# Optimization experiments

Measured on AMD Instinct MI355X. Metric: run time of the kernel, lower is better.

The kernel has to match this reference:

```python
import jax, jax.numpy as jnp
import numpy as np

TOP_K = 2


def setup_inputs() -> dict:
    key = jax.random.key(0)
    k1, k2, k3, k4 = jax.random.split(key, 4)
    B, T, D = 1, 2048, 1024
    E, F = 8, 2048
    scale_in = 1.0 / np.sqrt(D)
    scale_f = 1.0 / np.sqrt(F)
    x = jax.random.normal(k1, (B, T, D), dtype=jnp.float32)
    Wr = jax.random.normal(k2, (E, D), dtype=jnp.float32) * scale_in  # router weight [E, D]
    W1 = jax.random.normal(k3, (E, F, D), dtype=jnp.float32) * scale_in  # fc1 weights stacked [E, F, D]
    W2 = jax.random.normal(k4, (E, D, F), dtype=jnp.float32) * scale_f  # fc2 weights stacked [E, D, F]
    return {"x": x, "Wr": Wr, "W1": W1, "W2": W2}


def reference(x, Wr, W1, W2):
    B, T, D = x.shape
    E = Wr.shape[0]
    xf = x.reshape(B * T, D)  # [N, D]
    N = xf.shape[0]

    # Router: softmax over experts, top-k gating, renormalized
    logits = xf @ Wr.T  # [N, E]
    probs = jax.nn.softmax(logits, axis=-1)
    top_vals, top_idx = jax.lax.top_k(probs, TOP_K)  # [N, K]
    top_vals = top_vals / jnp.sum(top_vals, axis=-1, keepdims=True)

    # Dense per-token gate matrix: gates[n, e] = sum_k top_vals[n,k] * (top_idx[n,k]==e)
    gates = jnp.zeros((N, E), dtype=x.dtype).at[
        jnp.arange(N)[:, None], top_idx
    ].add(top_vals)  # [N, E]

    # Expert MLP: fc2(relu(fc1(x))^2), computed densely for all experts then
    # combined with the (mostly-zero) gate weights.
    h = jnp.einsum("nd,efd->nef", xf, W1)  # [N, E, F]
    a = jnp.square(jax.nn.relu(h))
    y = jnp.einsum("nef,edf->ned", a, W2)  # [N, E, D]
    out = jnp.einsum("ne,ned->nd", gates, y)  # [N, D]
    return out.reshape(B, T, D)
```

## Files before the change

### kernel.cpp

```cpp
#include <hip/hip_runtime.h>
#include <hip/hip_bf16.h>
#include <cstdint>
#include <cstddef>

#define N_TOK 2048
#define DIM   1024
#define NEXP  8
#define FDIM  2048

#define BM 128
#define BN 128
#define BK 64

typedef __attribute__((ext_vector_type(8))) short short8;
typedef __attribute__((ext_vector_type(4))) float f32x4;
typedef unsigned short ushort_t;

#define OFF_COUNTS  0
#define OFF_TOK     4096
#define OFF_GATE    (OFF_TOK + NEXP * N_TOK * 4)
#define OFF_A       ((size_t)1 << 20)
#define OFF_W1B     (OFF_A  + (size_t)2 * N_TOK * FDIM * 2)
#define OFF_W2B     (OFF_W1B + (size_t)NEXP * FDIM * DIM * 2)
#define OFF_XB      (OFF_W2B + (size_t)NEXP * DIM * FDIM * 2)

__device__ __forceinline__ uint32_t cvt2(float lo, float hi) {
  __hip_bfloat162 p = __float22bfloat162_rn(make_float2(lo, hi));
  uint32_t r; __builtin_memcpy(&r, &p, 4); return r;
}

__device__ __forceinline__ void gl16(const ushort_t* g, const ushort_t* l) {
  __builtin_amdgcn_global_load_lds(
      (const __attribute__((address_space(1))) void*)g,
      (__attribute__((address_space(3))) void*)l, 16, 0, 0);
}

__device__ __forceinline__ int xcd_swz(int bid, int nwg) {
  int q = nwg >> 3, r = nwg & 7;
  int xcd = bid & 7, local = bid >> 3;
  int base = (xcd < r) ? xcd * (q + 1) : r * (q + 1) + (xcd - r) * q;
  return base + local;
}

__global__ __launch_bounds__(256) void prep_kernel(
    const float* __restrict__ W1, const float* __restrict__ W2, const float* __restrict__ x,
    ushort_t* __restrict__ W1b, ushort_t* __restrict__ W2b, ushort_t* __restrict__ xb) {
  int b = blockIdx.x;
  const float* s; ushort_t* d; size_t off;
  if (b < 1024)      { s = W1; d = W1b; off = (size_t)b * 16384; }
  else if (b < 2048) { s = W2; d = W2b; off = (size_t)(b - 1024) * 16384; }
  else               { s = x;  d = xb;  off = (size_t)(b - 2048) * 16384; }
  s += off; d += off;
  int t8 = threadIdx.x * 8;
#pragma unroll
  for (int j = 0; j < 8; ++j) {
    float4 f0 = *(const float4*)(s + j * 2048 + t8);
    float4 f1 = *(const float4*)(s + j * 2048 + t8 + 4);
    *(uint4*)(d + j * 2048 + t8) =
        make_uint4(cvt2(f0.x, f0.y), cvt2(f0.z, f0.w), cvt2(f1.x, f1.y), cvt2(f1.z, f1.w));
  }
}

__global__ __launch_bounds__(256) void router_kernel(
    const float* __restrict__ x, const float* __restrict__ Wr,
    int* __restrict__ counts, int* __restrict__ toklist,
    float* __restrict__ gatelist) {
  int n = blockIdx.x * 4 + (threadIdx.x >> 6);
  int lane = threadIdx.x & 63;
  const float* xr = x + (size_t)n * DIM;

  float xv[DIM / 64];
#pragma unroll
  for (int i = 0; i < DIM / 64; ++i) xv[i] = xr[lane + 64 * i];

  float logit[NEXP];
#pragma unroll
  for (int e = 0; e < NEXP; ++e) {
    const float* wr = Wr + (size_t)e * DIM;
    float s = 0.f;
#pragma unroll
    for (int i = 0; i < DIM / 64; ++i) s += xv[i] * wr[lane + 64 * i];
#pragma unroll
    for (int off = 32; off; off >>= 1) s += __shfl_down(s, off);
    logit[e] = s;
  }

  if (lane == 0) {
    float m = logit[0];
#pragma unroll
    for (int e = 1; e < NEXP; ++e) m = fmaxf(m, logit[e]);
    float p[NEXP];
#pragma unroll
    for (int e = 0; e < NEXP; ++e) p[e] = expf(logit[e] - m);
    int i1 = 0;
#pragma unroll
    for (int e = 1; e < NEXP; ++e) if (p[e] > p[i1]) i1 = e;
    int i2 = (i1 == 0) ? 1 : 0;
#pragma unroll
    for (int e = 0; e < NEXP; ++e)
      if (e != i1 && p[e] > p[i2]) i2 = e;
    float denom = p[i1] + p[i2];

    int pos1 = atomicAdd(&counts[i1], 1);
    toklist[i1 * N_TOK + pos1] = n;
    gatelist[i1 * N_TOK + pos1] = p[i1] / denom;

    int pos2 = atomicAdd(&counts[i2], 1);
    toklist[i2 * N_TOK + pos2] = n;
    gatelist[i2 * N_TOK + pos2] = p[i2] / denom;
  }
}

__global__ __launch_bounds__(256, 3) void fc1_mfma(
    const ushort_t* __restrict__ xb, const ushort_t* __restrict__ W1b,
    const int* __restrict__ counts, const int* __restrict__ toklist,
    __hip_bfloat16* __restrict__ Abuf) {
  const int ROWB = N_TOK / BM;
  const int COLB = FDIM / BN;
  int bid = xcd_swz(blockIdx.x, NEXP * ROWB * COLB);
  int e  = bid / (ROWB * COLB);
  int rb = (bid / COLB) % ROWB;
  int cb = bid % COLB;
  int ne = counts[e];
  if (rb * BM >= ne) return;
  int base = 0;
  for (int i = 0; i < e; ++i) base += counts[i];

  __shared__ ushort_t As[BM * BK];
  __shared__ ushort_t Bs[BN * BK];

  int tid = threadIdx.x, lane = tid & 63, w = tid >> 6;

  const ushort_t* gA[4]; const ushort_t* gB[4];
  const ushort_t* lA[4]; const ushort_t* lB[4];
#pragma unroll
  for (int i = 0; i < 4; ++i) {
    int row = w * 32 + i * 8 + (lane >> 3);
    int c16 = (lane & 7) ^ (row & 7);
    int r = rb * BM + row; if (r >= ne) r = ne - 1;
    int tok = toklist[e * N_TOK + r];
    gA[i] = xb + (size_t)tok * DIM + c16 * 8;
    gB[i] = W1b + ((size_t)e * FDIM + cb * BN + row) * DIM + c16 * 8;
    lA[i] = &As[w * 2048 + i * 512];
    lB[i] = &Bs[w * 2048 + i * 512];
  }

  int wr = (w >> 1) * 64, wc = (w & 1) * 64;
  int lr = lane & 15, lg = lane >> 4;
  f32x4 acc[4][4] = {};

  for (int t = 0; t < DIM / BK; ++t) {
    __syncthreads();
#pragma unroll
    for (int i = 0; i < 4; ++i) {
      gl16(gA[i], lA[i]); gl16(gB[i], lB[i]);
      gA[i] += BK; gB[i] += BK;
    }
    __syncthreads();
#pragma unroll
    for (int ks = 0; ks < 2; ++ks) {
      short8 af[4], bf[4];
#pragma unroll
      for (int m = 0; m < 4; ++m) {
        int row = wr + m * 16 + lr;
        af[m] = *(const short8*)&As[row * BK + (((ks * 4 + lg) ^ (row & 7)) * 8)];
      }
#pragma unroll
      for (int n = 0; n < 4; ++n) {
        int row = wc + n * 16 + lr;
        bf[n] = *(const short8*)&Bs[row * BK + (((ks * 4 + lg) ^ (row & 7)) * 8)];
      }
#pragma unroll
      for (int m = 0; m < 4; ++m)
#pragma unroll
        for (int n = 0; n < 4; ++n)
          acc[m][n] = __builtin_amdgcn_mfma_f32_16x16x32_bf16(af[m], bf[n], acc[m][n], 0, 0, 0);
    }
  }

  int colbase = cb * BN + wc + lr;
#pragma unroll
  for (int m = 0; m < 4; ++m) {
#pragma unroll
    for (int j = 0; j < 4; ++j) {
      int r = rb * BM + wr + m * 16 + lg * 4 + j;
      if (r < ne) {
        __hip_bfloat16* orow = Abuf + (size_t)(base + r) * FDIM + colbase;
#pragma unroll
        for (int n = 0; n < 4; ++n) {
          float v = fmaxf(acc[m][n][j], 0.f);
          orow[n * 16] = __float2bfloat16(v * v);
        }
      }
    }
  }
}

__global__ __launch_bounds__(256, 3) void fc2_mfma(
    const ushort_t* __restrict__ Abuf, const ushort_t* __restrict__ W2b,
    const int* __restrict__ counts, const int* __restrict__ toklist,
    const float* __restrict__ gatelist, float* __restrict__ out) {
  const int ROWB = N_TOK / BM;
  const int COLB = DIM / BN;
  int bid = xcd_swz(blockIdx.x, NEXP * ROWB * COLB);
  int e  = bid / (ROWB * COLB);
  int rb = (bid / COLB) % ROWB;
  int cb = bid % COLB;
  int ks0 = blockIdx.y * (FDIM / 2);
  int ne = counts[e];
  if (rb * BM >= ne) return;
  int base = 0;
  for (int i = 0; i < e; ++i) base += counts[i];

  __shared__ ushort_t As[BM * BK];
  __shared__ ushort_t Bs[BN * BK];

  int tid = threadIdx.x, lane = tid & 63, w = tid >> 6;

  const ushort_t* gA[4]; const ushort_t* gB[4];
  const ushort_t* lA[4]; const ushort_t* lB[4];
#pragma unroll
  for (int i = 0; i < 4; ++i) {
    int row = w * 32 + i * 8 + (lane >> 3);
    int c16 = (lane & 7) ^ (row & 7);
    int r = rb * BM + row; if (r >= ne) r = ne - 1;
    gA[i] = Abuf + (size_t)(base + r) * FDIM + ks0 + c16 * 8;
    gB[i] = W2b + ((size_t)e * DIM + cb * BN + row) * FDIM + ks0 + c16 * 8;
    lA[i] = &As[w * 2048 + i * 512];
    lB[i] = &Bs[w * 2048 + i * 512];
  }

  int wr = (w >> 1) * 64, wc = (w & 1) * 64;
  int lr = lane & 15, lg = lane >> 4;
  f32x4 acc[4][4] = {};

  for (int t = 0; t < (FDIM / 2) / BK; ++t) {
    __syncthreads();
#pragma unroll
    for (int i = 0; i < 4; ++i) {
      gl16(gA[i], lA[i]); gl16(gB[i], lB[i]);
      gA[i] += BK; gB[i] += BK;
    }
    __syncthreads();
#pragma unroll
    for (int ks = 0; ks < 2; ++ks) {
      short8 af[4], bf[4];
#pragma unroll
      for (int m = 0; m < 4; ++m) {
        int row = wr + m * 16 + lr;
        af[m] = *(const short8*)&As[row * BK + (((ks * 4 + lg) ^ (row & 7)) * 8)];
      }
#pragma unroll
      for (int n = 0; n < 4; ++n) {
        int row = wc + n * 16 + lr;
        bf[n] = *(const short8*)&Bs[row * BK + (((ks * 4 + lg) ^ (row & 7)) * 8)];
      }
#pragma unroll
      for (int m = 0; m < 4; ++m)
#pragma unroll
        for (int n = 0; n < 4; ++n)
          acc[m][n] = __builtin_amdgcn_mfma_f32_16x16x32_bf16(af[m], bf[n], acc[m][n], 0, 0, 0);
    }
  }

  int colbase = cb * BN + wc + lr;
#pragma unroll
  for (int m = 0; m < 4; ++m) {
#pragma unroll
    for (int j = 0; j < 4; ++j) {
      int r = rb * BM + wr + m * 16 + lg * 4 + j;
      if (r < ne) {
        int tok = toklist[e * N_TOK + r];
        float g = gatelist[e * N_TOK + r];
        float* orow = out + (size_t)tok * DIM + colbase;
#pragma unroll
        for (int n = 0; n < 4; ++n)
          atomicAdd(&orow[n * 16], g * acc[m][n][j]);
      }
    }
  }
}

extern "C" void kernel_launch(void* const* d_in, const int* in_sizes, int n_in,
                              void* d_out, int out_size, void* d_ws, size_t ws_size,
                              hipStream_t stream) {
  const float* x  = (const float*)d_in[0];
  const float* Wr = (const float*)d_in[1];
  const float* W1 = (const float*)d_in[2];
  const float* W2 = (const float*)d_in[3];
  float* out = (float*)d_out;

  char* ws = (char*)d_ws;
  int*   counts   = (int*)(ws + OFF_COUNTS);
  int*   toklist  = (int*)(ws + OFF_TOK);
  float* gatelist = (float*)(ws + OFF_GATE);
  __hip_bfloat16* Abuf = (__hip_bfloat16*)(ws + OFF_A);
  ushort_t* W1b = (ushort_t*)(ws + OFF_W1B);
  ushort_t* W2b = (ushort_t*)(ws + OFF_W2B);
  ushort_t* xb  = (ushort_t*)(ws + OFF_XB);

  (void)hipMemsetAsync(counts, 0, NEXP * sizeof(int), stream);
  (void)hipMemsetAsync(out, 0, (size_t)out_size * sizeof(float), stream);

  prep_kernel<<<2176, 256, 0, stream>>>(W1, W2, x, W1b, W2b, xb);

  router_kernel<<<N_TOK / 4, 256, 0, stream>>>(x, Wr, counts, toklist, gatelist);

  fc1_mfma<<<NEXP * (N_TOK / BM) * (FDIM / BN), 256, 0, stream>>>(
      xb, W1b, counts, toklist, Abuf);

  fc2_mfma<<<dim3(NEXP * (N_TOK / BM) * (DIM / BN), 2), 256, 0, stream>>>(
      (const ushort_t*)Abuf, W2b, counts, toklist, gatelist, out);
}
```

Baseline: 295.5 us.

## Double-buffer LDS in expert GEMMs and split weight conversion into smaller blocks

Both fc1 and fc2 GEMM kernels now use two LDS buffers. The next K-tile is loaded asynchronously with global_load_lds while the current one is consumed, using explicit vmcnt waits and raw barriers instead of two __syncthreads per iteration. This is meant to hide global-load latency behind MFMA work, at the cost of doubling LDS per block, and the occupancy hint drops from 3 to 2 blocks. The fp32-to-bf16 prep kernel is also reorganized into twice as many blocks with nontemporal vector loads and 8-byte stores, aiming for better streaming bandwidth on the large weight conversion.

```diff
diff --git a/kernel.cpp b/kernel.cpp
--- a/kernel.cpp
+++ b/kernel.cpp
@@ -14,6 +14,7 @@
 
 typedef __attribute__((ext_vector_type(8))) short short8;
 typedef __attribute__((ext_vector_type(4))) float f32x4;
+typedef __attribute__((ext_vector_type(2))) unsigned int uint2v;
 typedef unsigned short ushort_t;
 
 #define OFF_COUNTS  0
@@ -46,18 +47,19 @@
     const float* __restrict__ W1, const float* __restrict__ W2, const float* __restrict__ x,
     ushort_t* __restrict__ W1b, ushort_t* __restrict__ W2b, ushort_t* __restrict__ xb) {
   int b = blockIdx.x;
-  const float* s; ushort_t* d; size_t off;
-  if (b < 1024)      { s = W1; d = W1b; off = (size_t)b * 16384; }
-  else if (b < 2048) { s = W2; d = W2b; off = (size_t)(b - 1024) * 16384; }
-  else               { s = x;  d = xb;  off = (size_t)(b - 2048) * 16384; }
+  const f32x4* s; uint2v* d; size_t off;
+  if (b < 2048)      { s = (const f32x4*)W1; d = (uint2v*)W1b; off = (size_t)b * 2048; }
+  else if (b < 4096) { s = (const f32x4*)W2; d = (uint2v*)W2b; off = (size_t)(b - 2048) * 2048; }
+  else               { s = (const f32x4*)x;  d = (uint2v*)xb;  off = (size_t)(b - 4096) * 2048; }
   s += off; d += off;
-  int t8 = threadIdx.x * 8;
-#pragma unroll
-  for (int j = 0; j < 8; ++j) {
-    float4 f0 = *(const float4*)(s + j * 2048 + t8);
-    float4 f1 = *(const float4*)(s + j * 2048 + t8 + 4);
-    *(uint4*)(d + j * 2048 + t8) =
-        make_uint4(cvt2(f0.x, f0.y), cvt2(f0.z, f0.w), cvt2(f1.x, f1.y), cvt2(f1.z, f1.w));
+  int tid = threadIdx.x;
+  f32x4 v[8];
+#pragma unroll
+  for (int k = 0; k < 8; ++k) v[k] = __builtin_nontemporal_load(&s[tid + k * 256]);
+#pragma unroll
+  for (int k = 0; k < 8; ++k) {
+    uint2v o; o.x = cvt2(v[k].x, v[k].y); o.y = cvt2(v[k].z, v[k].w);
+    d[tid + k * 256] = o;
   }
 }
 
@@ -111,7 +113,7 @@
   }
 }
 
-__global__ __launch_bounds__(256, 3) void fc1_mfma(
+__global__ __launch_bounds__(256, 2) void fc1_mfma(
     const ushort_t* __restrict__ xb, const ushort_t* __restrict__ W1b,
     const int* __restrict__ counts, const int* __restrict__ toklist,
     __hip_bfloat16* __restrict__ Abuf) {
@@ -126,13 +128,12 @@
   int base = 0;
   for (int i = 0; i < e; ++i) base += counts[i];
 
-  __shared__ ushort_t As[BM * BK];
-  __shared__ ushort_t Bs[BN * BK];
+  __shared__ ushort_t As[2][BM * BK];
+  __shared__ ushort_t Bs[2][BN * BK];
 
   int tid = threadIdx.x, lane = tid & 63, w = tid >> 6;
 
   const ushort_t* gA[4]; const ushort_t* gB[4];
-  const ushort_t* lA[4]; const ushort_t* lB[4];
 #pragma unroll
   for (int i = 0; i < 4; ++i) {
     int row = w * 32 + i * 8 + (lane >> 3);
@@ -141,34 +142,41 @@
     int tok = toklist[e * N_TOK + r];
     gA[i] = xb + (size_t)tok * DIM + c16 * 8;
     gB[i] = W1b + ((size_t)e * FDIM + cb * BN + row) * DIM + c16 * 8;
-    lA[i] = &As[w * 2048 + i * 512];
-    lB[i] = &Bs[w * 2048 + i * 512];
   }
 
   int wr = (w >> 1) * 64, wc = (w & 1) * 64;
   int lr = lane & 15, lg = lane >> 4;
   f32x4 acc[4][4] = {};
 
-  for (int t = 0; t < DIM / BK; ++t) {
-    __syncthreads();
-#pragma unroll
-    for (int i = 0; i < 4; ++i) {
-      gl16(gA[i], lA[i]); gl16(gB[i], lB[i]);
-      gA[i] += BK; gB[i] += BK;
-    }
-    __syncthreads();
+#define ISSUE(buf, t) do { _Pragma("unroll") for (int i = 0; i < 4; ++i) { \
+    gl16(gA[i] + (size_t)(t) * BK, &As[buf][w * 2048 + i * 512]); \
+    gl16(gB[i] + (size_t)(t) * BK, &Bs[buf][w * 2048 + i * 512]); } } while (0)
+
+  const int NT = DIM / BK;
+  asm volatile("s_waitcnt vmcnt(0)" ::: "memory");
+  ISSUE(0, 0);
+  for (int t = 0; t < NT; ++t) {
+    int cur = t & 1;
+    if (t + 1 < NT) {
+      ISSUE(cur ^ 1, t + 1);
+      asm volatile("s_waitcnt vmcnt(8)" ::: "memory");
+    } else {
+      asm volatile("s_waitcnt vmcnt(0)" ::: "memory");
+    }
+    __builtin_amdgcn_sched_barrier(0);
+    __builtin_amdgcn_s_barrier();
 #pragma unroll
     for (int ks = 0; ks < 2; ++ks) {
       short8 af[4], bf[4];
 #pragma unroll
       for (int m = 0; m < 4; ++m) {
         int row = wr + m * 16 + lr;
-        af[m] = *(const short8*)&As[row * BK + (((ks * 4 + lg) ^ (row & 7)) * 8)];
+        af[m] = *(const short8*)&As[cur][row * BK + (((ks * 4 + lg) ^ (row & 7)) * 8)];
       }
 #pragma unroll
       for (int n = 0; n < 4; ++n) {
         int row = wc + n * 16 + lr;
-        bf[n] = *(const short8*)&Bs[row * BK + (((ks * 4 + lg) ^ (row & 7)) * 8)];
+        bf[n] = *(const short8*)&Bs[cur][row * BK + (((ks * 4 + lg) ^ (row & 7)) * 8)];
       }
 #pragma unroll
       for (int m = 0; m < 4; ++m)
@@ -176,7 +184,11 @@
         for (int n = 0; n < 4; ++n)
           acc[m][n] = __builtin_amdgcn_mfma_f32_16x16x32_bf16(af[m], bf[n], acc[m][n], 0, 0, 0);
     }
-  }
+    asm volatile("s_waitcnt lgkmcnt(0)" ::: "memory");
+    __builtin_amdgcn_sched_barrier(0);
+    __builtin_amdgcn_s_barrier();
+  }
+#undef ISSUE
 
   int colbase = cb * BN + wc + lr;
 #pragma unroll
@@ -196,7 +208,7 @@
   }
 }
 
-__global__ __launch_bounds__(256, 3) void fc2_mfma(
+__global__ __launch_bounds__(256, 2) void fc2_mfma(
     const ushort_t* __restrict__ Abuf, const ushort_t* __restrict__ W2b,
     const int* __restrict__ counts, const int* __restrict__ toklist,
     const float* __restrict__ gatelist, float* __restrict__ out) {
@@ -212,13 +224,12 @@
   int base = 0;
   for (int i = 0; i < e; ++i) base += counts[i];
 
-  __shared__ ushort_t As[BM * BK];
-  __shared__ ushort_t Bs[BN * BK];
+  __shared__ ushort_t As[2][BM * BK];
+  __shared__ ushort_t Bs[2][BN * BK];
 
   int tid = threadIdx.x, lane = tid & 63, w = tid >> 6;
 
   const ushort_t* gA[4]; const ushort_t* gB[4];
-  const ushort_t* lA[4]; const ushort_t* lB[4];
 #pragma unroll
   for (int i = 0; i < 4; ++i) {
     int row = w * 32 + i * 8 + (lane >> 3);
@@ -226,34 +237,41 @@
     int r = rb * BM + row; if (r >= ne) r = ne - 1;
     gA[i] = Abuf + (size_t)(base + r) * FDIM + ks0 + c16 * 8;
     gB[i] = W2b + ((size_t)e * DIM + cb * BN + row) * FDIM + ks0 + c16 * 8;
-    lA[i] = &As[w * 2048 + i * 512];
-    lB[i] = &Bs[w * 2048 + i * 512];
   }
 
   int wr = (w >> 1) * 64, wc = (w & 1) * 64;
   int lr = lane & 15, lg = lane >> 4;
   f32x4 acc[4][4] = {};
 
-  for (int t = 0; t < (FDIM / 2) / BK; ++t) {
-    __syncthreads();
-#pragma unroll
-    for (int i = 0; i < 4; ++i) {
-      gl16(gA[i], lA[i]); gl16(gB[i], lB[i]);
-      gA[i] += BK; gB[i] += BK;
-    }
-    __syncthreads();
+#define ISSUE(buf, t) do { _Pragma("unroll") for (int i = 0; i < 4; ++i) { \
+    gl16(gA[i] + (size_t)(t) * BK, &As[buf][w * 2048 + i * 512]); \
+    gl16(gB[i] + (size_t)(t) * BK, &Bs[buf][w * 2048 + i * 512]); } } while (0)
+
+  const int NT = (FDIM / 2) / BK;
+  asm volatile("s_waitcnt vmcnt(0)" ::: "memory");
+  ISSUE(0, 0);
+  for (int t = 0; t < NT; ++t) {
+    int cur = t & 1;
+    if (t + 1 < NT) {
+      ISSUE(cur ^ 1, t + 1);
+      asm volatile("s_waitcnt vmcnt(8)" ::: "memory");
+    } else {
+      asm volatile("s_waitcnt vmcnt(0)" ::: "memory");
+    }
+    __builtin_amdgcn_sched_barrier(0);
+    __builtin_amdgcn_s_barrier();
 #pragma unroll
     for (int ks = 0; ks < 2; ++ks) {
       short8 af[4], bf[4];
 #pragma unroll
       for (int m = 0; m < 4; ++m) {
         int row = wr + m * 16 + lr;
-        af[m] = *(const short8*)&As[row * BK + (((ks * 4 + lg) ^ (row & 7)) * 8)];
+        af[m] = *(const short8*)&As[cur][row * BK + (((ks * 4 + lg) ^ (row & 7)) * 8)];
       }
 #pragma unroll
       for (int n = 0; n < 4; ++n) {
         int row = wc + n * 16 + lr;
-        bf[n] = *(const short8*)&Bs[row * BK + (((ks * 4 + lg) ^ (row & 7)) * 8)];
+        bf[n] = *(const short8*)&Bs[cur][row * BK + (((ks * 4 + lg) ^ (row & 7)) * 8)];
       }
 #pragma unroll
       for (int m = 0; m < 4; ++m)
@@ -261,7 +279,11 @@
         for (int n = 0; n < 4; ++n)
           acc[m][n] = __builtin_amdgcn_mfma_f32_16x16x32_bf16(af[m], bf[n], acc[m][n], 0, 0, 0);
     }
-  }
+    asm volatile("s_waitcnt lgkmcnt(0)" ::: "memory");
+    __builtin_amdgcn_sched_barrier(0);
+    __builtin_amdgcn_s_barrier();
+  }
+#undef ISSUE
 
   int colbase = cb * BN + wc + lr;
 #pragma unroll
@@ -302,7 +324,7 @@
   (void)hipMemsetAsync(counts, 0, NEXP * sizeof(int), stream);
   (void)hipMemsetAsync(out, 0, (size_t)out_size * sizeof(float), stream);
 
-  prep_kernel<<<2176, 256, 0, stream>>>(W1, W2, x, W1b, W2b, xb);
+  prep_kernel<<<4352, 256, 0, stream>>>(W1, W2, x, W1b, W2b, xb);
 
   router_kernel<<<N_TOK / 4, 256, 0, stream>>>(x, Wr, counts, toklist, gatelist);
 
```

Measured after the change: 307.0 us. 1.04x slower.
